# Performance work log

Hardware: AMD Instinct MI355X
Metric: run time of the kernel (lower is better)

The kernel has to match this reference:

```python
import jax, jax.numpy as jnp
from jax import lax
import numpy as np

# ---- config (matches init_kwargs) ----
B, T, D_IN = 4, 2048, 513
NC = D_IN - 1                 # neural channels
N_DAYS, N_CLASSES = 24, 41
PATCH, STRIDE = 14, 4
T_OUT = (T - PATCH) // STRIDE + 1   # 509
D_MODEL = 512                 # n_units
PROJ = 4096
L = 5                         # n_layers
DSTATE, DCONV, HEADDIM = 64, 4, 64
DI = 2 * D_MODEL              # expand=2 -> d_inner
H = DI // HEADDIM             # 16 heads
CONVD = DI + 2 * DSTATE       # conv channels (x,B,C)
DINPROJ = 2 * DI + 2 * DSTATE + H
NM = 2 * L                    # fwd+bwd Mamba instances
EPS = 1e-5


def setup_inputs() -> dict:
    key = jax.random.key(0)
    ks = jax.random.split(key, 16)
    s = 0.02
    x = jax.random.normal(ks[0], (B, T, D_IN), jnp.float32)
    day_idx = jax.random.randint(ks[1], (B,), 0, N_DAYS)
    day_w = jnp.eye(NC)[None] + s * jax.random.normal(ks[2], (N_DAYS, NC, NC), jnp.float32)
    day_b = s * jax.random.normal(ks[3], (N_DAYS, NC), jnp.float32)
    w1 = s * jax.random.normal(ks[4], (PROJ, D_IN * PATCH), jnp.float32)
    b1 = jnp.zeros((PROJ,), jnp.float32)
    w2 = s * jax.random.normal(ks[5], (D_MODEL, PROJ), jnp.float32)
    b2 = jnp.zeros((D_MODEL,), jnp.float32)
    ln_w = jnp.ones((L, D_MODEL), jnp.float32)
    ln_b = jnp.zeros((L, D_MODEL), jnp.float32)
    m_in_w = s * jax.random.normal(ks[6], (NM, DINPROJ, D_MODEL), jnp.float32)
    m_conv_w = s * jax.random.normal(ks[7], (NM, CONVD, DCONV), jnp.float32)
    m_conv_b = jnp.zeros((NM, CONVD), jnp.float32)
    dt = jax.random.uniform(ks[8], (NM, H), jnp.float32, 0.025, 1.0)
    m_dt = jnp.log(jnp.expm1(dt)) + 1.0          # dt_bias with +1 short-memory bias
    m_Alog = jnp.tile(jnp.log(jnp.arange(1, H + 1, dtype=jnp.float32))[None], (NM, 1))
    m_D = jnp.ones((NM, H), jnp.float32)
    m_norm_w = jnp.ones((NM, DI), jnp.float32)
    m_out_w = s * jax.random.normal(ks[9], (NM, D_MODEL, DI), jnp.float32)
    out_w = s * jax.random.normal(ks[10], (N_CLASSES, D_MODEL), jnp.float32)
    out_b = jnp.zeros((N_CLASSES,), jnp.float32)
    return dict(x=x, day_idx=day_idx, day_w=day_w, day_b=day_b, w1=w1, b1=b1,
                w2=w2, b2=b2, ln_w=ln_w, ln_b=ln_b, m_in_w=m_in_w, m_conv_w=m_conv_w,
                m_conv_b=m_conv_b, m_dt=m_dt, m_Alog=m_Alog, m_D=m_D,
                m_norm_w=m_norm_w, m_out_w=m_out_w, out_w=out_w, out_b=out_b)


def _layernorm(x, w, b):
    mu = jnp.mean(x, -1, keepdims=True)
    v = jnp.mean((x - mu) ** 2, -1, keepdims=True)
    return (x - mu) * lax.rsqrt(v + EPS) * w + b


def _mamba2(x, in_w, conv_w, conv_b, dt_bias, A_log, Dp, norm_w, out_w):
    """Mamba2 forward: x [B,T,Dm] -> [B,T,Dm]. Sequential selective scan."""
    Bn, Tn, _ = x.shape
    zxbcdt = x @ in_w.T                                   # [B,T,DINPROJ]
    z = zxbcdt[..., :DI]
    xBC = zxbcdt[..., DI:DI + CONVD]
    dt = jax.nn.softplus(zxbcdt[..., DI + CONVD:] + dt_bias)  # [B,T,H]
    # causal depthwise conv over time
    xc = jnp.transpose(xBC, (0, 2, 1))                    # [B,C,T]
    xc = lax.conv_general_dilated(xc, conv_w[:, None, :], (1,), [(DCONV - 1, 0)],
                                  feature_group_count=CONVD)
    xBC = jax.nn.silu(jnp.transpose(xc, (0, 2, 1)) + conv_b)
    xs = xBC[..., :DI].reshape(Bn, Tn, H, HEADDIM)        # [B,T,H,P]
    Bm = xBC[..., DI:DI + DSTATE]                         # [B,T,N] (ngroups=1)
    Cm = xBC[..., DI + DSTATE:]                           # [B,T,N]
    A = -jnp.exp(A_log)                                   # [H]
    dA = jnp.exp(dt * A)                                  # [B,T,H]

    def step(h, inp):
        xt, bt, ct, dat, dtt = inp                        # [B,H,P],[B,N],[B,N],[B,H],[B,H]
        h = h * dat[:, :, None, None] + (dtt[:, :, None] * xt)[..., None] * bt[:, None, None, :]
        y = jnp.einsum('bhpn,bn->bhp', h, ct)
        return h, y

    h0 = jnp.zeros((Bn, H, HEADDIM, DSTATE), x.dtype)
    xsT = jnp.moveaxis(xs, 1, 0)
    _, ys = lax.scan(step, h0, (xsT, jnp.moveaxis(Bm, 1, 0), jnp.moveaxis(Cm, 1, 0),
                                jnp.moveaxis(dA, 1, 0), jnp.moveaxis(dt, 1, 0)))
    y = jnp.moveaxis(ys, 0, 1) + Dp[None, None, :, None] * xs
    y = y.reshape(Bn, Tn, DI)
    y = y * jax.nn.silu(z)                                # gated RMSNorm
    y = y * lax.rsqrt(jnp.mean(y * y, -1, keepdims=True) + EPS) * norm_w
    return y @ out_w.T


def reference(x, day_idx, day_w, day_b, w1, b1, w2, b2, ln_w, ln_b,
              m_in_w, m_conv_w, m_conv_b, m_dt, m_Alog, m_D, m_norm_w, m_out_w,
              out_w, out_b):
    xn, xt = x[..., :-1], x[..., -1:]
    W = day_w[day_idx]                                    # [B,NC,NC]
    bsel = day_b[day_idx][:, None, :]
    xn = jnp.einsum('btd,bdk->btk', xn, W) + bsel
    xn = xn / (1.0 + jnp.abs(xn))                         # Softsign
    h = jnp.concatenate([xn, xt], -1)                     # [B,T,D_IN]
    # patch unfold: [B,T_OUT,PATCH,D_IN] -> [B,T_OUT,PATCH*D_IN]
    idx = jnp.arange(T_OUT)[:, None] * STRIDE + jnp.arange(PATCH)[None, :]
    h = h[:, idx, :].reshape(B, T_OUT, PATCH * D_IN)
    # input projection with Softsign
    h = h @ w1.T + b1
    h = h / (1.0 + jnp.abs(h))
    h = h @ w2.T + b2                                     # [B,T_OUT,D_MODEL]
    for i in range(L):
        hn = _layernorm(h, ln_w[i], ln_b[i])
        f, bw = 2 * i, 2 * i + 1
        of = _mamba2(hn, m_in_w[f], m_conv_w[f], m_conv_b[f], m_dt[f], m_Alog[f],
                     m_D[f], m_norm_w[f], m_out_w[f])
        ob = _mamba2(jnp.flip(hn, 1), m_in_w[bw], m_conv_w[bw], m_conv_b[bw], m_dt[bw],
                     m_Alog[bw], m_D[bw], m_norm_w[bw], m_out_w[bw])
        h = h + of + jnp.flip(ob, 1)
    return h @ out_w.T + out_b                            # [B,T_OUT,N_CLASSES]
```

## Files before the change

### kernel.cpp

```cpp
#include <hip/hip_runtime.h>

#define TB 4
#define TT 2048
#define DIN 513
#define TOUT 509
#define M2 2036
#define DM 512
#define PR 4096
#define DIc 1024
#define Hh 16
#define CONVD 1152
#define DINP 2192
#define ZLD 4384
#define LC 128
#define NC 4
#define KW1 7182
#define KP1 7200

typedef __attribute__((ext_vector_type(8))) short s8v;
typedef __attribute__((ext_vector_type(4))) float f4v;

__device__ __forceinline__ short f2b(float f) {
    unsigned u = __float_as_uint(f);
    u += 0x7fffu + ((u >> 16) & 1u);
    return (short)(u >> 16);
}

__device__ __forceinline__ void gld16(const void* g, void* l) {
    __builtin_amdgcn_global_load_lds(
        (const __attribute__((address_space(1))) unsigned int*)g,
        (__attribute__((address_space(3))) unsigned int*)l, 16, 0, 0);
}
__device__ __forceinline__ void gld4(const void* g, void* l) {
    __builtin_amdgcn_global_load_lds(
        (const __attribute__((address_space(1))) unsigned int*)g,
        (__attribute__((address_space(3))) unsigned int*)l, 4, 0, 0);
}

__global__ __launch_bounds__(256) void day_gemm(const float* __restrict__ x,
                                                const int* __restrict__ day_idx,
                                                const float* __restrict__ day_w,
                                                const float* __restrict__ day_b,
                                                short* __restrict__ hfull) {
    int b = blockIdx.z;
    int day = day_idx[b];
    int n0 = blockIdx.x * 64, m0 = blockIdx.y * 64;
    int tid = threadIdx.x;
    __shared__ float As[16][68], Bs[16][68];
    float acc[4][4] = {};
    int tm = tid >> 4, tn = tid & 15;
    int lrow = tid >> 2, lk = (tid & 3) * 4;
    const float* Ab = x + ((size_t)b * TT + m0) * DIN;
    const float* Bb = day_w + (size_t)day * 512 * 512;
    for (int k0 = 0; k0 < 512; k0 += 16) {
        #pragma unroll
        for (int j = 0; j < 4; j++)
            As[lk + j][lrow] = Ab[(size_t)lrow * DIN + k0 + lk + j];
        int kb = tid >> 4; int nb = (tid & 15) * 4;
        #pragma unroll
        for (int j = 0; j < 4; j++)
            Bs[kb][nb + j] = Bb[(size_t)(k0 + kb) * 512 + n0 + nb + j];
        __syncthreads();
        #pragma unroll
        for (int kk = 0; kk < 16; kk++) {
            float4 av = *(const float4*)&As[kk][tm * 4];
            float4 bv = *(const float4*)&Bs[kk][tn * 4];
            float a[4] = {av.x, av.y, av.z, av.w};
            float bb2[4] = {bv.x, bv.y, bv.z, bv.w};
            #pragma unroll
            for (int i = 0; i < 4; i++)
                #pragma unroll
                for (int j = 0; j < 4; j++) acc[i][j] += a[i] * bb2[j];
        }
        __syncthreads();
    }
    #pragma unroll
    for (int i = 0; i < 4; i++) {
        int m = m0 + tm * 4 + i;
        #pragma unroll
        for (int j = 0; j < 4; j++) {
            int n = n0 + tn * 4 + j;
            float v = acc[i][j] + day_b[day * 512 + n];
            v = v / (1.f + fabsf(v));
            hfull[((size_t)b * TT + m) * DIN + n] = f2b(v);
        }
    }
}

__global__ void copy_xt(const float* __restrict__ x, short* __restrict__ hfull) {
    int idx = blockIdx.x * 256 + threadIdx.x;
    if (idx >= TB * TT) return;
    hfull[(size_t)idx * DIN + 512] = f2b(x[(size_t)idx * DIN + 512]);
}

__global__ void cvt_w1(const float* __restrict__ s, short* __restrict__ d) {
    long idx = (long)blockIdx.x * 256 + threadIdx.x;
    if (idx >= (long)4096 * 900) return;
    int row = (int)(idx / 900);
    int kc = (int)(idx % 900) * 8;
    const float* src = s + (long)row * KW1 + kc;
    short* dst = d + (long)row * KP1 + kc;
    if (kc + 8 <= KW1) {
        const float2* s2 = (const float2*)src;
        #pragma unroll
        for (int j = 0; j < 4; j++) {
            float2 u = s2[j];
            dst[2 * j] = f2b(u.x); dst[2 * j + 1] = f2b(u.y);
        }
    } else {
        #pragma unroll
        for (int j = 0; j < 8; j++)
            dst[j] = (kc + j < KW1) ? f2b(src[j]) : (short)0;
    }
}

__global__ void cvtk(const float* __restrict__ s, short* __restrict__ d, long n) {
    long i = ((long)blockIdx.x * 256 + threadIdx.x) * 4;
    if (i >= n) return;
    float4 v = *(const float4*)(s + i);
    d[i] = f2b(v.x); d[i + 1] = f2b(v.y); d[i + 2] = f2b(v.z); d[i + 3] = f2b(v.w);
}

__global__ void cvt_outw(const float* __restrict__ fw, const float* __restrict__ bw,
                         short* __restrict__ d) {
    long idx = (long)blockIdx.x * 256 + threadIdx.x;
    if (idx >= (long)512 * 512) return;
    long e = idx * 4;
    int n = (int)(e >> 11);
    int k = (int)(e & 2047);
    const float* src = (k < 1024) ? (fw + (long)n * 1024 + k)
                                  : (bw + (long)n * 1024 + (k - 1024));
    float4 v = *(const float4*)src;
    short* dst = d + e;
    dst[0] = f2b(v.x); dst[1] = f2b(v.y); dst[2] = f2b(v.z); dst[3] = f2b(v.w);
}

template <int ACT, int ACCUM, int OUTBF, int AW>
__global__ __launch_bounds__(256) void bgemm(const short* __restrict__ A,
                                             const short* __restrict__ Bw,
                                             const float* __restrict__ bias,
                                             void* __restrict__ Cout,
                                             int M, int N, int K,
                                             int rowDiv, long sOuter, long sInner, int ldc) {
    __shared__ short As[128 * 32];
    __shared__ short Bs[128 * 32];
    int m0 = blockIdx.y * 128, n0 = blockIdx.x * 128;
    int tid = threadIdx.x;
    int wave = tid >> 6, lane = tid & 63;
    int wm = (wave & 1) * 64, wn = (wave >> 1) * 64;
    int lm = lane & 15, quad = lane >> 4;

    const short* Ap[(AW == 4) ? 8 : 2];
    if constexpr (AW == 4) {
        int kcc = (lane & 15) * 2;
        #pragma unroll
        for (int c = 0; c < 8; c++) {
            int r = m0 + wave * 32 + c * 4 + (lane >> 4);
            r = min(r, M - 1);
            Ap[c] = A + (long)(r / rowDiv) * sOuter + (long)(r % rowDiv) * sInner + kcc;
        }
    } else {
        int kca = (lane & 3) * 8;
        int r0 = min(m0 + wave * 32 + (lane >> 2), M - 1);
        int r1 = min(m0 + wave * 32 + 16 + (lane >> 2), M - 1);
        Ap[0] = A + (long)(r0 / rowDiv) * sOuter + (long)(r0 % rowDiv) * sInner + kca;
        Ap[1] = A + (long)(r1 / rowDiv) * sOuter + (long)(r1 % rowDiv) * sInner + kca;
    }
    int kcb = (lane & 3) * 8;
    int b0 = min(n0 + wave * 32 + (lane >> 2), N - 1);
    int b1 = min(n0 + wave * 32 + 16 + (lane >> 2), N - 1);
    const short* Bp0 = Bw + (long)b0 * K + kcb;
    const short* Bp1 = Bw + (long)b1 * K + kcb;
    short* lA = As + wave * 1024;
    short* lB = Bs + wave * 1024;

    f4v acc[4][4];
    #pragma unroll
    for (int i = 0; i < 4; i++)
        #pragma unroll
        for (int j = 0; j < 4; j++) acc[i][j] = (f4v){0.f, 0.f, 0.f, 0.f};

    for (int k0 = 0; k0 < K; k0 += 32) {
        if constexpr (AW == 4) {
            #pragma unroll
            for (int c = 0; c < 8; c++)
                gld4(Ap[c] + k0, lA + c * 128);
        } else {
            gld16(Ap[0] + k0, lA);
            gld16(Ap[1] + k0, lA + 512);
        }
        gld16(Bp0 + k0, lB);
        gld16(Bp1 + k0, lB + 512);
        __syncthreads();
        s8v af[4], bf[4];
        #pragma unroll
        for (int i = 0; i < 4; i++)
            af[i] = *(const s8v*)&As[(wm + i * 16 + lm) * 32 + quad * 8];
        #pragma unroll
        for (int j = 0; j < 4; j++)
            bf[j] = *(const s8v*)&Bs[(wn + j * 16 + lm) * 32 + quad * 8];
        #pragma unroll
        for (int i = 0; i < 4; i++)
            #pragma unroll
            for (int j = 0; j < 4; j++)
                acc[i][j] = __builtin_amdgcn_mfma_f32_16x16x32_bf16(af[i], bf[j], acc[i][j], 0, 0, 0);
        __syncthreads();
    }

    #pragma unroll
    for (int i = 0; i < 4; i++) {
        #pragma unroll
        for (int e = 0; e < 4; e++) {
            int m = m0 + wm + i * 16 + quad * 4 + e;
            if (m >= M) continue;
            #pragma unroll
            for (int j = 0; j < 4; j++) {
                int n = n0 + wn + j * 16 + lm;
                if (n >= N) continue;
                float v = acc[i][j][e];
                if (bias) v += bias[n];
                if (ACT == 1) v = v / (1.f + fabsf(v));
                long ci = (long)m * ldc + n;
                if constexpr (OUTBF) {
                    ((short*)Cout)[ci] = f2b(v);
                } else {
                    float* Cf = (float*)Cout;
                    if constexpr (ACCUM) v += Cf[ci];
                    Cf[ci] = v;
                }
            }
        }
    }
}

__global__ __launch_bounds__(64) void ln_kernel(const float* __restrict__ h,
                                                const float* __restrict__ w,
                                                const float* __restrict__ bgain,
                                                short* __restrict__ hn) {
    int m = blockIdx.x, lane = threadIdx.x;
    const float* row = h + (size_t)m * DM;
    float v[8]; float s = 0.f;
    #pragma unroll
    for (int j = 0; j < 8; j++) { v[j] = row[lane + j * 64]; s += v[j]; }
    for (int o = 1; o < 64; o <<= 1) s += __shfl_xor(s, o);
    float mu = s * (1.f / DM);
    float var = 0.f;
    #pragma unroll
    for (int j = 0; j < 8; j++) { float d = v[j] - mu; var += d * d; }
    for (int o = 1; o < 64; o <<= 1) var += __shfl_xor(var, o);
    float inv = rsqrtf(var * (1.f / DM) + 1e-5f);
    #pragma unroll
    for (int j = 0; j < 8; j++) {
        int c = lane + j * 64;
        hn[(size_t)m * DM + c] = f2b((v[j] - mu) * inv * w[c] + bgain[c]);
    }
}

__global__ void conv_kernel(const float* __restrict__ zx2,
                            const float* __restrict__ cw,
                            const float* __restrict__ cb,
                            float* __restrict__ xbcc) {
    int idx = blockIdx.x * 256 + threadIdx.x;
    if (idx >= 2 * M2 * CONVD) return;
    int dir = idx / (M2 * CONVD);
    int r = idx - dir * (M2 * CONVD);
    int m = r / CONVD; int c = r - m * CONVD;
    int b = m / TOUT; int t = m - b * TOUT;
    float acc = cb[dir * CONVD + c];
    const float* w = cw + (size_t)(dir * CONVD + c) * 4;
    #pragma unroll
    for (int k = 0; k < 4; k++) {
        int tp = dir ? (t + 3 - k) : (t - 3 + k);
        if (tp >= 0 && tp < TOUT)
            acc += w[k] * zx2[(size_t)(b * TOUT + tp) * ZLD + dir * DINP + DIc + c];
    }
    xbcc[(size_t)idx] = acc / (1.f + expf(-acc));
}

__global__ void dt_kernel(const float* __restrict__ zx2,
                          const float* __restrict__ dtB,
                          const float* __restrict__ alog,
                          float* __restrict__ dtb, float* __restrict__ dab) {
    int idx = blockIdx.x * 256 + threadIdx.x;
    if (idx >= 2 * M2 * Hh) return;
    int dir = idx / (M2 * Hh);
    int r = idx - dir * (M2 * Hh);
    int m = r / Hh; int hh = r - m * Hh;
    float raw = zx2[(size_t)m * ZLD + dir * DINP + DIc + CONVD + hh] + dtB[dir * Hh + hh];
    float sp = raw > 20.f ? raw : log1pf(expf(raw));
    float A = -expf(alog[dir * Hh + hh]);
    dtb[idx] = sp;
    dab[idx] = expf(sp * A);
}

__global__ __launch_bounds__(64) void scan_local(const float* __restrict__ xbcc,
                                                 const float* __restrict__ dtb,
                                                 const float* __restrict__ dab,
                                                 const float* __restrict__ Dp_pair,
                                                 float* __restrict__ ybuf,
                                                 float* __restrict__ Hbuf,
                                                 float* __restrict__ Pcum) {
    int h = blockIdx.x & 15, chunk = blockIdx.x >> 4;
    int b = blockIdx.y, dir = blockIdx.z;
    int lane = threadIdx.x;
    int s0 = chunk * LC;
    int s1 = min(s0 + LC, TOUT);
    __shared__ __align__(16) float bsh[2][64];
    __shared__ __align__(16) float csh[2][64];
    float st[64];
    #pragma unroll
    for (int n = 0; n < 64; n++) st[n] = 0.f;
    float Dpv = Dp_pair[dir * Hh + h];
    const float* xb = xbcc + (size_t)dir * M2 * CONVD;
    long dtbase = (size_t)(dir * M2 + b * TOUT) * Hh + h;
    int id = (dir * TB + b) * Hh + h;
    float* pcm = Pcum + (size_t)id * TOUT;

    int tt0 = dir ? (TOUT - 1 - s0) : s0;
    const float* row0 = xb + (size_t)(b * TOUT + tt0) * CONVD;
    float bcur = row0[DIc + lane];
    float ccur = row0[DIc + 64 + lane];
    float xcur = row0[h * 64 + lane];
    float dtcur = dtb[dtbase + (long)tt0 * Hh];
    float dacur = dab[dtbase + (long)tt0 * Hh];
    float P = 1.f;

    for (int s = s0; s < s1; s++) {
        int pb = s & 1;
        bsh[pb][lane] = bcur;
        csh[pb][lane] = ccur;
        float xp = xcur, dtt = dtcur, da = dacur;
        __syncthreads();
        if (s + 1 < s1) {
            int tn = dir ? (TOUT - 1 - (s + 1)) : (s + 1);
            const float* rown = xb + (size_t)(b * TOUT + tn) * CONVD;
            bcur = rown[DIc + lane];
            ccur = rown[DIc + 64 + lane];
            xcur = rown[h * 64 + lane];
            dtcur = dtb[dtbase + (long)tn * Hh];
            dacur = dab[dtbase + (long)tn * Hh];
        }
        float common = dtt * xp;
        float y0 = 0.f, y1 = 0.f, y2 = 0.f, y3 = 0.f;
        #pragma unroll
        for (int n4 = 0; n4 < 16; n4++) {
            float4 bv = ((const float4*)bsh[pb])[n4];
            float4 cv = ((const float4*)csh[pb])[n4];
            int n = n4 * 4;
            st[n]     = st[n]     * da + common * bv.x; y0 += st[n]     * cv.x;
            st[n + 1] = st[n + 1] * da + common * bv.y; y1 += st[n + 1] * cv.y;
            st[n + 2] = st[n + 2] * da + common * bv.z; y2 += st[n + 2] * cv.z;
            st[n + 3] = st[n + 3] * da + common * bv.w; y3 += st[n + 3] * cv.w;
        }
        int tt = dir ? (TOUT - 1 - s) : s;
        int m = b * TOUT + tt;
        ybuf[((size_t)dir * M2 + m) * DIc + h * 64 + lane] = (y0 + y1) + (y2 + y3) + Dpv * xp;
        P *= da;
        if (lane == 0) pcm[s] = P;
    }
    float* Ho = Hbuf + (((size_t)id * NC + chunk) * 64 + lane) * 64;
    #pragma unroll
    for (int n4 = 0; n4 < 16; n4++) {
        ((float4*)Ho)[n4] = (float4){st[n4 * 4], st[n4 * 4 + 1], st[n4 * 4 + 2], st[n4 * 4 + 3]};
    }
}

__global__ __launch_bounds__(64) void scan_combine(float* __restrict__ Hbuf,
                                                   const float* __restrict__ Pcum) {
    int id = blockIdx.x;
    int lane = threadIdx.x;
    float Hin[64];
    #pragma unroll
    for (int n = 0; n < 64; n++) Hin[n] = 0.f;
    const float* pcm = Pcum + (size_t)id * TOUT;
    for (int c = 0; c < NC; c++) {
        float* Hp = Hbuf + (((size_t)id * NC + c) * 64 + lane) * 64;
        float Hout[64];
        #pragma unroll
        for (int n4 = 0; n4 < 16; n4++) {
            float4 v = ((const float4*)Hp)[n4];
            Hout[n4 * 4] = v.x; Hout[n4 * 4 + 1] = v.y;
            Hout[n4 * 4 + 2] = v.z; Hout[n4 * 4 + 3] = v.w;
        }
        #pragma unroll
        for (int n4 = 0; n4 < 16; n4++)
            ((float4*)Hp)[n4] = (float4){Hin[n4 * 4], Hin[n4 * 4 + 1], Hin[n4 * 4 + 2], Hin[n4 * 4 + 3]};
        int send = min((c + 1) * LC, TOUT) - 1;
        float Pe = pcm[send];
        #pragma unroll
        for (int n = 0; n < 64; n++) Hin[n] = Hout[n] + Pe * Hin[n];
    }
}

__global__ __launch_bounds__(64) void scan_fix(const float* __restrict__ xbcc,
                                               const float* __restrict__ Hbuf,
                                               const float* __restrict__ Pcum,
                                               float* __restrict__ ybuf) {
    int h = blockIdx.x & 15;
    int q = (blockIdx.x >> 4) & 3;
    int c = 1 + (blockIdx.x >> 6);
    int b = blockIdx.y, dir = blockIdx.z, lane = threadIdx.x;
    int s0 = c * LC;
    int s1 = min(s0 + LC, TOUT);
    int sa = s0 + q * (LC / 4);
    int se = min(sa + LC / 4, s1);
    if (sa >= se) return;
    int id = (dir * TB + b) * Hh + h;
    float Hr[64];
    const float* Hp = Hbuf + (((size_t)id * NC + c) * 64 + lane) * 64;
    #pragma unroll
    for (int n4 = 0; n4 < 16; n4++) {
        float4 v = ((const float4*)Hp)[n4];
        Hr[n4 * 4] = v.x; Hr[n4 * 4 + 1] = v.y; Hr[n4 * 4 + 2] = v.z; Hr[n4 * 4 + 3] = v.w;
    }
    const float* pcm = Pcum + (size_t)id * TOUT;
    const float* xb = xbcc + (size_t)dir * M2 * CONVD;
    for (int s = sa; s < se; s++) {
        int tt = dir ? (TOUT - 1 - s) : s;
        const float4* crow = (const float4*)(xb + (size_t)(b * TOUT + tt) * CONVD + DIc + 64);
        float acc = 0.f;
        #pragma unroll
        for (int n4 = 0; n4 < 16; n4++) {
            float4 cv = crow[n4];
            acc += Hr[n4 * 4] * cv.x + Hr[n4 * 4 + 1] * cv.y
                 + Hr[n4 * 4 + 2] * cv.z + Hr[n4 * 4 + 3] * cv.w;
        }
        size_t yi = ((size_t)dir * M2 + b * TOUT + tt) * DIc + h * 64 + lane;
        ybuf[yi] += pcm[s] * acc;
    }
}

__global__ __launch_bounds__(64) void grms_kernel(const float* __restrict__ ybuf,
                                                  const float* __restrict__ zx2,
                                                  const float* __restrict__ nw,
                                                  short* __restrict__ yo) {
    int m = blockIdx.x, dir = blockIdx.y, lane = threadIdx.x;
    const float* y = ybuf + ((size_t)dir * M2 + m) * DIc;
    const float* z = zx2 + (size_t)m * ZLD + dir * DINP;
    float g[16]; float ss = 0.f;
    #pragma unroll
    for (int j = 0; j < 16; j++) {
        int c = lane + j * 64;
        float zv = z[c];
        float gv = y[c] * (zv / (1.f + expf(-zv)));
        g[j] = gv; ss += gv * gv;
    }
    for (int o = 1; o < 64; o <<= 1) ss += __shfl_xor(ss, o);
    float sc = rsqrtf(ss * (1.f / DIc) + 1e-5f);
    #pragma unroll
    for (int j = 0; j < 16; j++) {
        int c = lane + j * 64;
        yo[(size_t)m * (2 * DIc) + dir * DIc + c] = f2b(g[j] * sc * nw[dir * DIc + c]);
    }
}

__global__ __launch_bounds__(64) void outk(const float* __restrict__ h,
                                           const float* __restrict__ ow,
                                           const float* __restrict__ ob,
                                           float* __restrict__ out) {
    int m = blockIdx.x, lane = threadIdx.x;
    __shared__ float hs[DM];
    #pragma unroll
    for (int j = 0; j < 8; j++) hs[lane + j * 64] = h[(size_t)m * DM + lane + j * 64];
    __syncthreads();
    if (lane < 41) {
        float acc = ob[lane];
        for (int d = 0; d < DM; d++) acc += hs[d] * ow[lane * DM + d];
        out[(size_t)m * 41 + lane] = acc;
    }
}

extern "C" void kernel_launch(void* const* d_in, const int* in_sizes, int n_in,
                              void* d_out, int out_size, void* d_ws, size_t ws_size,
                              hipStream_t stream) {
    const float* x        = (const float*)d_in[0];
    const int*   day_idx  = (const int*)d_in[1];
    const float* day_w    = (const float*)d_in[2];
    const float* day_b    = (const float*)d_in[3];
    const float* w1       = (const float*)d_in[4];
    const float* b1       = (const float*)d_in[5];
    const float* w2       = (const float*)d_in[6];
    const float* b2       = (const float*)d_in[7];
    const float* ln_w     = (const float*)d_in[8];
    const float* ln_b     = (const float*)d_in[9];
    const float* m_in_w   = (const float*)d_in[10];
    const float* m_conv_w = (const float*)d_in[11];
    const float* m_conv_b = (const float*)d_in[12];
    const float* m_dt     = (const float*)d_in[13];
    const float* m_Alog   = (const float*)d_in[14];
    const float* m_D      = (const float*)d_in[15];
    const float* m_norm_w = (const float*)d_in[16];
    const float* m_out_w  = (const float*)d_in[17];
    const float* out_w    = (const float*)d_in[18];
    const float* out_b    = (const float*)d_in[19];

    float* ws = (float*)d_ws;
    float* zx2  = ws;
    float* xbcc = ws + 8925824;
    short* ybf  = (short*)(ws + 8925824);
    float* ybuf = ws + 13616768;
    float* Hbuf = ws + 17786496;
    float* Pcum = ws + 19883648;
    float* dtb  = ws + 19948800;
    float* dab  = ws + 20013952;
    short* inwb = (short*)(ws + 20079104);
    short* outwb= (short*)(ws + 21201408);
    short* hfb  = (short*)ws;
    short* B1   = (short*)(ws + 2103296);
    short* h1b  = (short*)(ws + 16848896);
    short* w2b  = (short*)(ws + 21018624);
    float* hbuf = ws + 22067200;
    short* hnb  = (short*)(ws + 23109632);

    day_gemm<<<dim3(8, 32, 4), 256, 0, stream>>>(x, day_idx, day_w, day_b, hfb);
    copy_xt<<<32, 256, 0, stream>>>(x, hfb);
    cvt_w1<<<14400, 256, 0, stream>>>(w1, B1);
    cvtk<<<2048, 256, 0, stream>>>(w2, w2b, (long)512 * PR);
    bgemm<1, 0, 1, 4><<<dim3(32, 16), 256, 0, stream>>>(hfb, B1, b1, h1b,
                                                        M2, PR, KP1, TOUT, (long)TT * DIN, (long)4 * DIN, PR);
    bgemm<0, 0, 0, 16><<<dim3(4, 16), 256, 0, stream>>>(h1b, w2b, b2, hbuf,
                                                        M2, DM, PR, 1, (long)PR, 0L, DM);
    for (int i = 0; i < 5; i++) {
        ln_kernel<<<M2, 64, 0, stream>>>(hbuf, ln_w + i * DM, ln_b + i * DM, hnb);
        cvtk<<<2192, 256, 0, stream>>>(m_in_w + (size_t)2 * i * DINP * DM, inwb, (long)2 * DINP * DM);
        bgemm<0, 0, 0, 16><<<dim3(35, 16), 256, 0, stream>>>(hnb, inwb, nullptr, zx2,
                                                             M2, ZLD, DM, 1, (long)DM, 0L, ZLD);
        conv_kernel<<<(2 * M2 * CONVD + 255) / 256, 256, 0, stream>>>(
            zx2, m_conv_w + (size_t)2 * i * CONVD * 4, m_conv_b + (size_t)2 * i * CONVD, xbcc);
        dt_kernel<<<(2 * M2 * Hh + 255) / 256, 256, 0, stream>>>(
            zx2, m_dt + 2 * i * Hh, m_Alog + 2 * i * Hh, dtb, dab);
        scan_local<<<dim3(Hh * NC, TB, 2), 64, 0, stream>>>(xbcc, dtb, dab, m_D + 2 * i * Hh,
                                                            ybuf, Hbuf, Pcum);
        scan_combine<<<128, 64, 0, stream>>>(Hbuf, Pcum);
        scan_fix<<<dim3(Hh * 4 * (NC - 1), TB, 2), 64, 0, stream>>>(xbcc, Hbuf, Pcum, ybuf);
        grms_kernel<<<dim3(M2, 2), 64, 0, stream>>>(ybuf, zx2, m_norm_w + (size_t)2 * i * DIc, ybf);
        cvt_outw<<<1024, 256, 0, stream>>>(m_out_w + (size_t)(2 * i) * DM * DIc,
                                           m_out_w + (size_t)(2 * i + 1) * DM * DIc, outwb);
        bgemm<0, 1, 0, 16><<<dim3(4, 16), 256, 0, stream>>>(ybf, outwb, nullptr, hbuf,
                                                            M2, DM, 2 * DIc, 1, (long)(2 * DIc), 0L, DM);
    }
    outk<<<M2, 64, 0, stream>>>(hbuf, out_w, out_b, (float*)d_out);
}
```

Before: 2.224 ms.

## Split-K with atomic accumulation for narrow GEMMs and XCD-aware block remapping

The narrow N=512 GEMMs (w2 projection and the Mamba out-projection) launched only 64 workgroups. They now split K four ways across gridDim.z and accumulate into the fp32 output with atomic adds. The bias is pre-filled by a new fillb kernel, and the out-projection's residual add is handled by accumulating atomically into hbuf. Block indices are also remapped so that consecutive tiles land on the same XCD, aiming for better L2 locality. This raises occupancy on the 256-CU device, at the cost of atomic traffic, non-deterministic summation order, and an extra fill launch.

```diff
diff --git a/kernel.cpp b/kernel.cpp
--- a/kernel.cpp
+++ b/kernel.cpp
@@ -135,7 +135,13 @@
     dst[0] = f2b(v.x); dst[1] = f2b(v.y); dst[2] = f2b(v.z); dst[3] = f2b(v.w);
 }
 
-template <int ACT, int ACCUM, int OUTBF, int AW>
+__global__ void fillb(float* __restrict__ dst, const float* __restrict__ b, int total, int N) {
+    int idx = blockIdx.x * 256 + threadIdx.x;
+    if (idx >= total) return;
+    dst[idx] = b[idx & (N - 1)];
+}
+
+template <int ACT, int ACCUM, int OUTBF, int ATOMIC, int AW>
 __global__ __launch_bounds__(256) void bgemm(const short* __restrict__ A,
                                              const short* __restrict__ Bw,
                                              const float* __restrict__ bias,
@@ -144,7 +150,14 @@
                                              int rowDiv, long sOuter, long sInner, int ldc) {
     __shared__ short As[128 * 32];
     __shared__ short Bs[128 * 32];
-    int m0 = blockIdx.y * 128, n0 = blockIdx.x * 128;
+    int nwg = gridDim.x * gridDim.y;
+    int orig = blockIdx.y * gridDim.x + blockIdx.x;
+    int q = nwg >> 3, rr = nwg & 7;
+    int xcd = orig & 7, ii = orig >> 3;
+    int wg = (xcd < rr ? xcd * (q + 1) : rr * (q + 1) + (xcd - rr) * q) + ii;
+    int bx = wg % gridDim.x, by = wg / gridDim.x;
+    int m0 = by * 128, n0 = bx * 128;
+
     int tid = threadIdx.x;
     int wave = tid >> 6, lane = tid & 63;
     int wm = (wave & 1) * 64, wn = (wave >> 1) * 64;
@@ -180,7 +193,9 @@
         #pragma unroll
         for (int j = 0; j < 4; j++) acc[i][j] = (f4v){0.f, 0.f, 0.f, 0.f};
 
-    for (int k0 = 0; k0 < K; k0 += 32) {
+    int kper = K, kbeg = 0;
+    if constexpr (ATOMIC) { kper = K / (int)gridDim.z; kbeg = blockIdx.z * kper; }
+    for (int k0 = kbeg; k0 < kbeg + kper; k0 += 32) {
         if constexpr (AW == 4) {
             #pragma unroll
             for (int c = 0; c < 8; c++)
@@ -223,6 +238,8 @@
                 long ci = (long)m * ldc + n;
                 if constexpr (OUTBF) {
                     ((short*)Cout)[ci] = f2b(v);
+                } else if constexpr (ATOMIC) {
+                    unsafeAtomicAdd(&((float*)Cout)[ci], v);
                 } else {
                     float* Cf = (float*)Cout;
                     if constexpr (ACCUM) v += Cf[ci];
@@ -495,6 +512,12 @@
     const float* out_b    = (const float*)d_in[19];
 
     float* ws = (float*)d_ws;
+    short* hfb  = (short*)ws;
+    short* B1   = (short*)(ws + 2103296);
+    short* h1b  = (short*)(ws + 16848896);
+    short* w2b  = (short*)(ws + 21018624);
+    float* hbuf = ws + 22067200;
+    short* hnb  = (short*)(ws + 23109632);
     float* zx2  = ws;
     float* xbcc = ws + 8925824;
     short* ybf  = (short*)(ws + 8925824);
@@ -505,26 +528,21 @@
     float* dab  = ws + 20013952;
     short* inwb = (short*)(ws + 20079104);
     short* outwb= (short*)(ws + 21201408);
-    short* hfb  = (short*)ws;
-    short* B1   = (short*)(ws + 2103296);
-    short* h1b  = (short*)(ws + 16848896);
-    short* w2b  = (short*)(ws + 21018624);
-    float* hbuf = ws + 22067200;
-    short* hnb  = (short*)(ws + 23109632);
 
     day_gemm<<<dim3(8, 32, 4), 256, 0, stream>>>(x, day_idx, day_w, day_b, hfb);
     copy_xt<<<32, 256, 0, stream>>>(x, hfb);
     cvt_w1<<<14400, 256, 0, stream>>>(w1, B1);
     cvtk<<<2048, 256, 0, stream>>>(w2, w2b, (long)512 * PR);
-    bgemm<1, 0, 1, 4><<<dim3(32, 16), 256, 0, stream>>>(hfb, B1, b1, h1b,
-                                                        M2, PR, KP1, TOUT, (long)TT * DIN, (long)4 * DIN, PR);
-    bgemm<0, 0, 0, 16><<<dim3(4, 16), 256, 0, stream>>>(h1b, w2b, b2, hbuf,
-                                                        M2, DM, PR, 1, (long)PR, 0L, DM);
+    bgemm<1, 0, 1, 0, 4><<<dim3(32, 16), 256, 0, stream>>>(
+        hfb, B1, b1, h1b, M2, PR, KP1, TOUT, (long)TT * DIN, (long)4 * DIN, PR);
+    fillb<<<(M2 * DM + 255) / 256, 256, 0, stream>>>(hbuf, b2, M2 * DM, DM);
+    bgemm<0, 0, 0, 1, 16><<<dim3(4, 16, 4), 256, 0, stream>>>(h1b, w2b, nullptr, hbuf,
+                                                              M2, DM, PR, 1, (long)PR, 0L, DM);
     for (int i = 0; i < 5; i++) {
         ln_kernel<<<M2, 64, 0, stream>>>(hbuf, ln_w + i * DM, ln_b + i * DM, hnb);
         cvtk<<<2192, 256, 0, stream>>>(m_in_w + (size_t)2 * i * DINP * DM, inwb, (long)2 * DINP * DM);
-        bgemm<0, 0, 0, 16><<<dim3(35, 16), 256, 0, stream>>>(hnb, inwb, nullptr, zx2,
-                                                             M2, ZLD, DM, 1, (long)DM, 0L, ZLD);
+        bgemm<0, 0, 0, 0, 16><<<dim3(35, 16), 256, 0, stream>>>(hnb, inwb, nullptr, zx2,
+                                                                M2, ZLD, DM, 1, (long)DM, 0L, ZLD);
         conv_kernel<<<(2 * M2 * CONVD + 255) / 256, 256, 0, stream>>>(
             zx2, m_conv_w + (size_t)2 * i * CONVD * 4, m_conv_b + (size_t)2 * i * CONVD, xbcc);
         dt_kernel<<<(2 * M2 * Hh + 255) / 256, 256, 0, stream>>>(
@@ -536,8 +554,8 @@
         grms_kernel<<<dim3(M2, 2), 64, 0, stream>>>(ybuf, zx2, m_norm_w + (size_t)2 * i * DIc, ybf);
         cvt_outw<<<1024, 256, 0, stream>>>(m_out_w + (size_t)(2 * i) * DM * DIc,
                                            m_out_w + (size_t)(2 * i + 1) * DM * DIc, outwb);
-        bgemm<0, 1, 0, 16><<<dim3(4, 16), 256, 0, stream>>>(ybf, outwb, nullptr, hbuf,
-                                                            M2, DM, 2 * DIc, 1, (long)(2 * DIc), 0L, DM);
+        bgemm<0, 0, 0, 1, 16><<<dim3(4, 16, 4), 256, 0, stream>>>(ybf, outwb, nullptr, hbuf,
+                                                                  M2, DM, 2 * DIc, 1, (long)(2 * DIc), 0L, DM);
     }
     outk<<<M2, 64, 0, stream>>>(hbuf, out_w, out_b, (float*)d_out);
 }
```

Measured after the change: 2.021 ms. -9.2%, faster.
